# Kernel tuning notes

Measured on AMD Instinct MI355X. Metric: run time of the kernel, lower is better.

Reference implementation:

```python
import jax, jax.numpy as jnp
import numpy as np

N_NODES = 50000
N_EDGES = 800000
N_FEAT = 128
N_HID = 128
N_CLS = 40
BN_EPS = 1e-5


def setup_inputs() -> dict:
    key = jax.random.key(0)
    ks = jax.random.split(key, 8)
    return {
        "x": jax.random.normal(ks[0], (N_NODES, N_FEAT), dtype=jnp.float32),
        "edge_index": jax.random.randint(ks[1], (2, N_EDGES), 0, N_NODES, dtype=jnp.int64),
        "W1l": jax.random.normal(ks[2], (N_HID, N_FEAT), dtype=jnp.float32) / np.sqrt(N_FEAT),
        "b1": jnp.zeros((N_HID,), dtype=jnp.float32),
        "W1r": jax.random.normal(ks[3], (N_HID, N_FEAT), dtype=jnp.float32) / np.sqrt(N_FEAT),
        "gamma": jnp.ones((N_HID,), dtype=jnp.float32),
        "beta": jnp.zeros((N_HID,), dtype=jnp.float32),
        "run_mean": jax.random.normal(ks[4], (N_HID,), dtype=jnp.float32) * 0.1,
        "run_var": jax.random.uniform(ks[5], (N_HID,), dtype=jnp.float32) + 0.5,
        "W2l": jax.random.normal(ks[6], (N_CLS, N_HID), dtype=jnp.float32) / np.sqrt(N_HID),
        "b2": jnp.zeros((N_CLS,), dtype=jnp.float32),
        "W2r": jax.random.normal(ks[7], (N_CLS, N_HID), dtype=jnp.float32) / np.sqrt(N_HID),
    }


def _sage_conv(h, src, dst, n_nodes, inv_deg, Wl, bl, Wr):
    # mean-aggregate neighbor features at each destination node
    agg = jax.ops.segment_sum(h[src], dst, num_segments=n_nodes)  # [N, D]
    agg = agg * inv_deg[:, None]
    # PyG SAGEConv: lin_l(aggr) (with bias) + lin_r(x) (no bias)
    return agg @ Wl.T + bl + h @ Wr.T


def reference(x, edge_index, W1l, b1, W1r, gamma, beta, run_mean, run_var, W2l, b2, W2r):
    src, dst = edge_index[0], edge_index[1]
    n = x.shape[0]
    deg = jax.ops.segment_sum(jnp.ones_like(src, dtype=x.dtype), dst, num_segments=n)
    inv_deg = 1.0 / jnp.maximum(deg, 1.0)
    h = _sage_conv(x, src, dst, n, inv_deg, W1l, b1, W1r)
    # transition: ReLU -> BatchNorm1d (eval: running stats) -> Dropout (identity in eval)
    h = jnp.maximum(h, 0.0)
    h = (h - run_mean) * (gamma / jnp.sqrt(run_var + BN_EPS)) + beta
    out = _sage_conv(h, src, dst, n, inv_deg, W2l, b2, W2r)
    return out
```

## Files before the change

### kernel.cpp

```cpp
#include <hip/hip_runtime.h>

#define N_NODES 50000
#define N_EDGES 800000
#define N_FEAT 128
#define N_HID 128
#define N_CLS 40
#define BN_EPS 1e-5f

#define CSR_STRIDE 64
#define NXCD 8
#define P_NODES 6250
#define CSR_B 1024
#define CSR_BO 128
#define WPACK_B 84
#define XPACK_B 3125

typedef short bf16x8 __attribute__((ext_vector_type(8)));
typedef float f32x4 __attribute__((ext_vector_type(4)));

__device__ __forceinline__ unsigned bfpack(float a, float b) {
    unsigned ua = __float_as_uint(a), ub = __float_as_uint(b);
    ua = (ua + 0x7FFFu + ((ua >> 16) & 1u)) >> 16;
    ub = (ub + 0x7FFFu + ((ub >> 16) & 1u)) >> 16;
    return ua | (ub << 16);
}
__device__ __forceinline__ unsigned short bfr1(float a) {
    unsigned u = __float_as_uint(a);
    u = (u + 0x7FFFu + ((u >> 16) & 1u)) >> 16;
    return (unsigned short)u;
}
__device__ __forceinline__ float bflo(unsigned u) { return __uint_as_float(u << 16); }
__device__ __forceinline__ float bfhi(unsigned u) { return __uint_as_float(u & 0xFFFF0000u); }

__global__ __launch_bounds__(256) void degprep_kernel(
    const int* __restrict__ src, const int* __restrict__ dst,
    int* __restrict__ deg_i, unsigned short* __restrict__ csr_pad,
    const float* __restrict__ W1l, const float* __restrict__ W1r,
    const float* __restrict__ W2l, const float* __restrict__ W2r,
    const float* __restrict__ x, unsigned* __restrict__ WfA,
    unsigned* __restrict__ WfB, unsigned* __restrict__ x_bf16) {
    int b = blockIdx.x;
    int t = threadIdx.x;
    if (b < CSR_B) {
        const int p = b & (NXCD - 1);
        const int bo = b >> 3;
        const int plo = p * P_NODES;
        const int phi = plo + P_NODES;
        const int4* dst4 = (const int4*)dst;
        const int4* src4 = (const int4*)src;
        for (int c = bo; c * 2048 < N_EDGES; c += CSR_BO) {
            int e = c * 2048 + t * 8;
            if (e < N_EDGES) {
                int i4 = e >> 2;
                int4 da = dst4[i4];
                int4 db = dst4[i4 + 1];
                bool ka0 = (da.x >= plo) && (da.x < phi);
                bool ka1 = (da.y >= plo) && (da.y < phi);
                bool ka2 = (da.z >= plo) && (da.z < phi);
                bool ka3 = (da.w >= plo) && (da.w < phi);
                bool kb0 = (db.x >= plo) && (db.x < phi);
                bool kb1 = (db.y >= plo) && (db.y < phi);
                bool kb2 = (db.z >= plo) && (db.z < phi);
                bool kb3 = (db.w >= plo) && (db.w < phi);
                int4 sa = {0, 0, 0, 0}, sb = {0, 0, 0, 0};
                if (ka0 | ka1 | ka2 | ka3) sa = src4[i4];
                if (kb0 | kb1 | kb2 | kb3) sb = src4[i4 + 1];
                if (ka0) { int r = atomicAdd(&deg_i[da.x], 1);
                    if (r < CSR_STRIDE) csr_pad[da.x * CSR_STRIDE + r] = (unsigned short)sa.x; }
                if (ka1) { int r = atomicAdd(&deg_i[da.y], 1);
                    if (r < CSR_STRIDE) csr_pad[da.y * CSR_STRIDE + r] = (unsigned short)sa.y; }
                if (ka2) { int r = atomicAdd(&deg_i[da.z], 1);
                    if (r < CSR_STRIDE) csr_pad[da.z * CSR_STRIDE + r] = (unsigned short)sa.z; }
                if (ka3) { int r = atomicAdd(&deg_i[da.w], 1);
                    if (r < CSR_STRIDE) csr_pad[da.w * CSR_STRIDE + r] = (unsigned short)sa.w; }
                if (kb0) { int r = atomicAdd(&deg_i[db.x], 1);
                    if (r < CSR_STRIDE) csr_pad[db.x * CSR_STRIDE + r] = (unsigned short)sb.x; }
                if (kb1) { int r = atomicAdd(&deg_i[db.y], 1);
                    if (r < CSR_STRIDE) csr_pad[db.y * CSR_STRIDE + r] = (unsigned short)sb.y; }
                if (kb2) { int r = atomicAdd(&deg_i[db.z], 1);
                    if (r < CSR_STRIDE) csr_pad[db.z * CSR_STRIDE + r] = (unsigned short)sb.z; }
                if (kb3) { int r = atomicAdd(&deg_i[db.w], 1);
                    if (r < CSR_STRIDE) csr_pad[db.w * CSR_STRIDE + r] = (unsigned short)sb.w; }
            }
        }
        return;
    }
    int i = (b - CSR_B) * 256 + t;
    if (b < CSR_B + WPACK_B) {
        if (i < 16384) {
            int f = i >> 8, r = i & 255;
            int lane = r >> 2, u = r & 3;
            int phase = f >> 5, kc = (f >> 3) & 3, nt = f & 7;
            int k0 = phase * 128 + kc * 32 + (lane >> 4) * 8 + u * 2;
            int n = nt * 16 + (lane & 15);
            float w0, w1;
            if (k0 < 128) {
                w0 = W1l[n * 128 + k0];
                w1 = W1l[n * 128 + k0 + 1];
            } else {
                w0 = W1r[n * 128 + k0 - 128];
                w1 = W1r[n * 128 + k0 - 127];
            }
            WfA[i] = bfpack(w0, w1);
        } else if (i < 21504) {
            int j = i - 16384;
            int f = j >> 8, r = j & 255;
            int lane = r >> 2, u = r & 3;
            int kc = f / 5, nt = f % 5;
            int k0 = kc * 32 + (lane >> 4) * 8 + u * 2;
            int n = nt * 16 + (lane & 15);
            float w0, w1;
            if (n < 40) {
                w0 = W2l[n * 128 + k0];
                w1 = W2l[n * 128 + k0 + 1];
            } else {
                w0 = W2r[(n - 40) * 128 + k0];
                w1 = W2r[(n - 40) * 128 + k0 + 1];
            }
            WfB[j] = bfpack(w0, w1);
        }
    } else {
        int j = (b - CSR_B - WPACK_B) * 256 + t;
        if (j < 800000) {
            const float4* xf = (const float4*)x;
            float4 a = xf[(size_t)j * 2];
            float4 bq = xf[(size_t)j * 2 + 1];
            uint4 o;
            o.x = bfpack(a.x, a.y);
            o.y = bfpack(a.z, a.w);
            o.z = bfpack(bq.x, bq.y);
            o.w = bfpack(bq.z, bq.w);
            ((uint4*)x_bf16)[j] = o;
        }
    }
}

__global__ __launch_bounds__(256) void gather1_kernel(const unsigned short* __restrict__ csr_pad,
                                                      const int* __restrict__ deg_i,
                                                      const unsigned* __restrict__ x_bf16,
                                                      unsigned* __restrict__ agg1b) {
    int sg = threadIdx.x >> 4;
    int li = threadIdx.x & 15;
    int gid = blockIdx.x * 16 + sg;
    if (gid >= N_NODES) return;
    int n = min(deg_i[gid], CSR_STRIDE);
    int beg = gid * CSR_STRIDE;
    int end = beg + n;
    const uint4* xb = (const uint4*)x_bf16;
    float acc[8];
#pragma unroll
    for (int j = 0; j < 8; ++j) acc[j] = 0.f;

    int e = beg;
    for (; e + 7 < end; e += 8) {
        uint4 tv[8];
#pragma unroll
        for (int q = 0; q < 8; ++q) {
            int s = csr_pad[e + q];
            tv[q] = xb[(size_t)s * 16 + li];
        }
#pragma unroll
        for (int q = 0; q < 8; ++q) {
            acc[0] += bflo(tv[q].x); acc[1] += bfhi(tv[q].x);
            acc[2] += bflo(tv[q].y); acc[3] += bfhi(tv[q].y);
            acc[4] += bflo(tv[q].z); acc[5] += bfhi(tv[q].z);
            acc[6] += bflo(tv[q].w); acc[7] += bfhi(tv[q].w);
        }
    }
    if (e + 3 < end) {
        uint4 tv[4];
#pragma unroll
        for (int q = 0; q < 4; ++q) {
            int s = csr_pad[e + q];
            tv[q] = xb[(size_t)s * 16 + li];
        }
#pragma unroll
        for (int q = 0; q < 4; ++q) {
            acc[0] += bflo(tv[q].x); acc[1] += bfhi(tv[q].x);
            acc[2] += bflo(tv[q].y); acc[3] += bfhi(tv[q].y);
            acc[4] += bflo(tv[q].z); acc[5] += bfhi(tv[q].z);
            acc[6] += bflo(tv[q].w); acc[7] += bfhi(tv[q].w);
        }
        e += 4;
    }
    for (; e < end; ++e) {
        int s = csr_pad[e];
        uint4 t0 = xb[(size_t)s * 16 + li];
        acc[0] += bflo(t0.x); acc[1] += bfhi(t0.x);
        acc[2] += bflo(t0.y); acc[3] += bfhi(t0.y);
        acc[4] += bflo(t0.z); acc[5] += bfhi(t0.z);
        acc[6] += bflo(t0.w); acc[7] += bfhi(t0.w);
    }
    float inv = 1.0f / fmaxf((float)n, 1.0f);
    uint4 o;
    o.x = bfpack(acc[0] * inv, acc[1] * inv);
    o.y = bfpack(acc[2] * inv, acc[3] * inv);
    o.z = bfpack(acc[4] * inv, acc[5] * inv);
    o.w = bfpack(acc[6] * inv, acc[7] * inv);
    ((uint4*)agg1b)[(size_t)gid * 16 + li] = o;
}

__global__ __launch_bounds__(256) void gemm_fused_kernel(
    const unsigned* __restrict__ agg1b, const unsigned* __restrict__ xb,
    const unsigned* __restrict__ WfA, const unsigned* __restrict__ WfB,
    const float* __restrict__ b1,
    const float* __restrict__ gamma, const float* __restrict__ beta,
    const float* __restrict__ rmean, const float* __restrict__ rvar,
    unsigned short* __restrict__ z2s, float* __restrict__ p2) {
    __shared__ unsigned Asu[64 * 68];
    const int t = threadIdx.x;
    const int wid = __builtin_amdgcn_readfirstlane(t >> 6);
    const int lane = t & 63;
    const int li = lane & 15;
    const int quad = lane >> 4;
    const int mbase = blockIdx.x * 64;

    f32x4 dacc[8];
#pragma unroll
    for (int nt = 0; nt < 8; ++nt) dacc[nt] = (f32x4){0.f, 0.f, 0.f, 0.f};

    for (int phase = 0; phase < 2; ++phase) {
        const unsigned* __restrict__ A = phase ? xb : agg1b;
        __syncthreads();
#pragma unroll
        for (int i = 0; i < 4; ++i) {
            int e = i * 256 + t;
            int row = e >> 4, seg = e & 15;
            int rr = mbase + row;
            rr = (rr < N_NODES) ? rr : N_NODES - 1;
            uint4 v = ((const uint4*)A)[(size_t)rr * 16 + seg];
            *(uint4*)&Asu[row * 68 + seg * 4] = v;
        }
        __syncthreads();
        bf16x8 af[4];
#pragma unroll
        for (int kc = 0; kc < 4; ++kc)
            af[kc] = *(const bf16x8*)&Asu[(wid * 16 + li) * 68 + kc * 16 + quad * 4];

        const unsigned* __restrict__ Wp = WfA + phase * 8192;
#pragma unroll
        for (int nt = 0; nt < 8; ++nt) {
#pragma unroll
            for (int kc = 0; kc < 4; ++kc) {
                bf16x8 bfr = *(const bf16x8*)(Wp + (size_t)(kc * 8 + nt) * 256 + lane * 4);
                dacc[nt] = __builtin_amdgcn_mfma_f32_16x16x32_bf16(af[kc], bfr, dacc[nt], 0, 0, 0);
            }
        }
    }

    __syncthreads();
    unsigned short* Hs = (unsigned short*)Asu;
#pragma unroll
    for (int nt = 0; nt < 8; ++nt) {
        int cg = nt * 16 + li;
        float sc = gamma[cg] * rsqrtf(rvar[cg] + BN_EPS);
        float sh = fmaf(-rmean[cg], sc, beta[cg]);
        float bb = b1[cg];
#pragma unroll
        for (int r = 0; r < 4; ++r) {
            int row = wid * 16 + quad * 4 + r;
            float pre = dacc[nt][r] + bb;
            Hs[row * 136 + cg] = bfr1(fmaf(fmaxf(pre, 0.f), sc, sh));
        }
    }
    __syncthreads();

    bf16x8 af2[4];
#pragma unroll
    for (int kc = 0; kc < 4; ++kc)
        af2[kc] = *(const bf16x8*)&Asu[(wid * 16 + li) * 68 + kc * 16 + quad * 4];

    f32x4 d2[5];
#pragma unroll
    for (int nt = 0; nt < 5; ++nt) d2[nt] = (f32x4){0.f, 0.f, 0.f, 0.f};
#pragma unroll
    for (int nt = 0; nt < 5; ++nt) {
#pragma unroll
        for (int kc = 0; kc < 4; ++kc) {
            bf16x8 bfr = *(const bf16x8*)(WfB + (size_t)(kc * 5 + nt) * 256 + lane * 4);
            d2[nt] = __builtin_amdgcn_mfma_f32_16x16x32_bf16(af2[kc], bfr, d2[nt], 0, 0, 0);
        }
    }

#pragma unroll
    for (int nt = 0; nt < 5; ++nt) {
        int cg = nt * 16 + li;
#pragma unroll
        for (int r = 0; r < 4; ++r) {
            int row = mbase + wid * 16 + quad * 4 + r;
            if (row < N_NODES) {
                float vv = d2[nt][r];
                if (cg < 40) z2s[(size_t)row * 40 + cg] = bfr1(vv);
                else p2[(size_t)row * 40 + (cg - 40)] = vv;
            }
        }
    }
}

__global__ __launch_bounds__(256) void gather2_kernel(const unsigned short* __restrict__ csr_pad,
                                                      const int* __restrict__ deg_i,
                                                      const unsigned short* __restrict__ z2s,
                                                      const float* __restrict__ p2,
                                                      const float* __restrict__ b2,
                                                      float* __restrict__ out) {
    int t = threadIdx.x;
    int sub = t / 10;
    int li = t - sub * 10;
    if (sub >= 25) return;
    int gid = blockIdx.x * 25 + sub;
    if (gid >= N_NODES) return;
    int n = min(deg_i[gid], CSR_STRIDE);
    int beg = gid * CSR_STRIDE;
    int end = beg + n;
    const uint2* z2 = (const uint2*)z2s;
    float4 acc = {0.f, 0.f, 0.f, 0.f};
    int e = beg;
    for (; e + 7 < end; e += 8) {
        uint2 tv[8];
#pragma unroll
        for (int q = 0; q < 8; ++q) {
            int s = csr_pad[e + q];
            tv[q] = z2[(size_t)s * 10 + li];
        }
#pragma unroll
        for (int q = 0; q < 8; ++q) {
            acc.x += bflo(tv[q].x); acc.y += bfhi(tv[q].x);
            acc.z += bflo(tv[q].y); acc.w += bfhi(tv[q].y);
        }
    }
    if (e + 3 < end) {
        uint2 tv[4];
#pragma unroll
        for (int q = 0; q < 4; ++q) {
            int s = csr_pad[e + q];
            tv[q] = z2[(size_t)s * 10 + li];
        }
#pragma unroll
        for (int q = 0; q < 4; ++q) {
            acc.x += bflo(tv[q].x); acc.y += bfhi(tv[q].x);
            acc.z += bflo(tv[q].y); acc.w += bfhi(tv[q].y);
        }
        e += 4;
    }
    for (; e < end; ++e) {
        int s = csr_pad[e];
        uint2 t0 = z2[(size_t)s * 10 + li];
        acc.x += bflo(t0.x); acc.y += bfhi(t0.x);
        acc.z += bflo(t0.y); acc.w += bfhi(t0.y);
    }
    float inv = 1.0f / fmaxf((float)n, 1.0f);
    float4 p = ((const float4*)p2)[(size_t)gid * 10 + li];
    float4 bb = ((const float4*)b2)[li];
    float4 r;
    r.x = fmaf(acc.x, inv, p.x + bb.x);
    r.y = fmaf(acc.y, inv, p.y + bb.y);
    r.z = fmaf(acc.z, inv, p.z + bb.z);
    r.w = fmaf(acc.w, inv, p.w + bb.w);
    ((float4*)out)[(size_t)gid * 10 + li] = r;
}

extern "C" void kernel_launch(void* const* d_in, const int* in_sizes, int n_in,
                              void* d_out, int out_size, void* d_ws, size_t ws_size,
                              hipStream_t stream) {
    const float* x     = (const float*)d_in[0];
    const int*   ei    = (const int*)d_in[1];
    const float* W1l   = (const float*)d_in[2];
    const float* b1    = (const float*)d_in[3];
    const float* W1r   = (const float*)d_in[4];
    const float* gamma = (const float*)d_in[5];
    const float* beta  = (const float*)d_in[6];
    const float* rmean = (const float*)d_in[7];
    const float* rvar  = (const float*)d_in[8];
    const float* W2l   = (const float*)d_in[9];
    const float* b2    = (const float*)d_in[10];
    const float* W2r   = (const float*)d_in[11];
    float* out = (float*)d_out;

    int* deg_i              = (int*)d_ws;
    unsigned short* csr_pad = (unsigned short*)(deg_i + 50048);
    unsigned* WfA           = (unsigned*)(deg_i + 50048 + 1600000);
    unsigned* WfB           = WfA + 16384;
    unsigned* x_bf16        = WfB + 5120;
    unsigned* agg1b         = x_bf16 + 3200000;
    unsigned short* z2s     = (unsigned short*)(agg1b + (size_t)50048 * 64);
    float* p2               = (float*)(z2s + (size_t)50048 * 40);

    const int* src = ei;
    const int* dst = ei + N_EDGES;

    hipMemsetAsync(deg_i, 0, (size_t)50048 * sizeof(int), stream);

    degprep_kernel<<<CSR_B + WPACK_B + XPACK_B, 256, 0, stream>>>(
        src, dst, deg_i, csr_pad, W1l, W1r, W2l, W2r, x, WfA, WfB, x_bf16);

    gather1_kernel<<<(N_NODES + 15) / 16, 256, 0, stream>>>(csr_pad, deg_i, x_bf16, agg1b);

    gemm_fused_kernel<<<(N_NODES + 63) / 64, 256, 0, stream>>>(
        agg1b, x_bf16, WfA, WfB, b1, gamma, beta, rmean, rvar, z2s, p2);

    gather2_kernel<<<(N_NODES + 24) / 25, 256, 0, stream>>>(csr_pad, deg_i, z2s, p2, b2, out);
}
```

Measured before the change: 195.5 us.

## Store bf16 features segment-major and partition gather1 segments across XCDs

The bf16 copy of x and the layer-1 aggregate are now stored as 16 feature segments, each 16 bytes wide and laid out contiguously over all nodes, instead of row-major per node. gather1 assigns one node-segment per thread, and blockIdx&7 selects the segment pair, so each XCD's blocks touch only two segments of x. The intent is that each XCD's working set fits in its own L2, cutting cross-die and HBM traffic for the random neighbor gathers. The cost is that each gathered load becomes an isolated 16-byte access instead of a coalesced 256-byte row read, so cache-line utilisation drops. The GEMM tile load is updated to read the new layout.

```diff
diff --git a/kernel.cpp b/kernel.cpp
--- a/kernel.cpp
+++ b/kernel.cpp
@@ -14,6 +14,8 @@
 #define CSR_BO 128
 #define WPACK_B 84
 #define XPACK_B 3125
+#define SEG_N 50048
+#define G1_OB 391
 
 typedef short bf16x8 __attribute__((ext_vector_type(8)));
 typedef float f32x4 __attribute__((ext_vector_type(4)));
@@ -122,15 +124,17 @@
     } else {
         int j = (b - CSR_B - WPACK_B) * 256 + t;
         if (j < 800000) {
+            int seg = j / 50000;
+            int node = j - seg * 50000;
             const float4* xf = (const float4*)x;
-            float4 a = xf[(size_t)j * 2];
-            float4 bq = xf[(size_t)j * 2 + 1];
+            float4 a = xf[(size_t)node * 32 + seg * 2];
+            float4 bq = xf[(size_t)node * 32 + seg * 2 + 1];
             uint4 o;
             o.x = bfpack(a.x, a.y);
             o.y = bfpack(a.z, a.w);
             o.z = bfpack(bq.x, bq.y);
             o.w = bfpack(bq.z, bq.w);
-            ((uint4*)x_bf16)[j] = o;
+            ((uint4*)x_bf16)[(size_t)seg * SEG_N + node] = o;
         }
     }
 }
@@ -139,14 +143,17 @@
                                                       const int* __restrict__ deg_i,
                                                       const unsigned* __restrict__ x_bf16,
                                                       unsigned* __restrict__ agg1b) {
-    int sg = threadIdx.x >> 4;
-    int li = threadIdx.x & 15;
-    int gid = blockIdx.x * 16 + sg;
-    if (gid >= N_NODES) return;
-    int n = min(deg_i[gid], CSR_STRIDE);
-    int beg = gid * CSR_STRIDE;
+    int b = blockIdx.x;
+    int g = b & 7;
+    int o = b >> 3;
+    int t = threadIdx.x;
+    int node = o * 128 + (t & 127);
+    int seg = g + ((t >> 7) << 3);
+    const uint4* xs = (const uint4*)x_bf16 + (size_t)seg * SEG_N;
+
+    int n = min(deg_i[node], CSR_STRIDE);
+    int beg = node * CSR_STRIDE;
     int end = beg + n;
-    const uint4* xb = (const uint4*)x_bf16;
     float acc[8];
 #pragma unroll
     for (int j = 0; j < 8; ++j) acc[j] = 0.f;
@@ -157,7 +164,7 @@
 #pragma unroll
         for (int q = 0; q < 8; ++q) {
             int s = csr_pad[e + q];
-            tv[q] = xb[(size_t)s * 16 + li];
+            tv[q] = xs[s];
         }
 #pragma unroll
         for (int q = 0; q < 8; ++q) {
@@ -172,7 +179,7 @@
 #pragma unroll
         for (int q = 0; q < 4; ++q) {
             int s = csr_pad[e + q];
-            tv[q] = xb[(size_t)s * 16 + li];
+            tv[q] = xs[s];
         }
 #pragma unroll
         for (int q = 0; q < 4; ++q) {
@@ -185,19 +192,19 @@
     }
     for (; e < end; ++e) {
         int s = csr_pad[e];
-        uint4 t0 = xb[(size_t)s * 16 + li];
+        uint4 t0 = xs[s];
         acc[0] += bflo(t0.x); acc[1] += bfhi(t0.x);
         acc[2] += bflo(t0.y); acc[3] += bfhi(t0.y);
         acc[4] += bflo(t0.z); acc[5] += bfhi(t0.z);
         acc[6] += bflo(t0.w); acc[7] += bfhi(t0.w);
     }
     float inv = 1.0f / fmaxf((float)n, 1.0f);
-    uint4 o;
-    o.x = bfpack(acc[0] * inv, acc[1] * inv);
-    o.y = bfpack(acc[2] * inv, acc[3] * inv);
-    o.z = bfpack(acc[4] * inv, acc[5] * inv);
-    o.w = bfpack(acc[6] * inv, acc[7] * inv);
-    ((uint4*)agg1b)[(size_t)gid * 16 + li] = o;
+    uint4 o4;
+    o4.x = bfpack(acc[0] * inv, acc[1] * inv);
+    o4.y = bfpack(acc[2] * inv, acc[3] * inv);
+    o4.z = bfpack(acc[4] * inv, acc[5] * inv);
+    o4.w = bfpack(acc[6] * inv, acc[7] * inv);
+    ((uint4*)agg1b)[(size_t)seg * SEG_N + node] = o4;
 }
 
 __global__ __launch_bounds__(256) void gemm_fused_kernel(
@@ -225,10 +232,10 @@
 #pragma unroll
         for (int i = 0; i < 4; ++i) {
             int e = i * 256 + t;
-            int row = e >> 4, seg = e & 15;
+            int seg = e >> 6, row = e & 63;
             int rr = mbase + row;
             rr = (rr < N_NODES) ? rr : N_NODES - 1;
-            uint4 v = ((const uint4*)A)[(size_t)rr * 16 + seg];
+            uint4 v = ((const uint4*)A)[(size_t)seg * SEG_N + rr];
             *(uint4*)&Asu[row * 68 + seg * 4] = v;
         }
         __syncthreads();
@@ -381,8 +388,8 @@
     unsigned* WfA           = (unsigned*)(deg_i + 50048 + 1600000);
     unsigned* WfB           = WfA + 16384;
     unsigned* x_bf16        = WfB + 5120;
-    unsigned* agg1b         = x_bf16 + 3200000;
-    unsigned short* z2s     = (unsigned short*)(agg1b + (size_t)50048 * 64);
+    unsigned* agg1b         = x_bf16 + (size_t)16 * SEG_N * 4;
+    unsigned short* z2s     = (unsigned short*)(agg1b + (size_t)16 * SEG_N * 4);
     float* p2               = (float*)(z2s + (size_t)50048 * 40);
 
     const int* src = ei;
@@ -393,7 +400,7 @@
     degprep_kernel<<<CSR_B + WPACK_B + XPACK_B, 256, 0, stream>>>(
         src, dst, deg_i, csr_pad, W1l, W1r, W2l, W2r, x, WfA, WfB, x_bf16);
 
-    gather1_kernel<<<(N_NODES + 15) / 16, 256, 0, stream>>>(csr_pad, deg_i, x_bf16, agg1b);
+    gather1_kernel<<<8 * G1_OB, 256, 0, stream>>>(csr_pad, deg_i, x_bf16, agg1b);
 
     gemm_fused_kernel<<<(N_NODES + 63) / 64, 256, 0, stream>>>(
         agg1b, x_bf16, WfA, WfB, b1, gamma, beta, rmean, rvar, z2s, p2);
```

Result: slower. 241.4 us (+23.5%).

## Fuse layer-1 gather into the dense GEMM kernel with 16-row tiles

Applied to the files above, without the earlier changes.

Merges the neighbor-mean gather and the fused two-GEMM/BN kernel into one kernel. Each 256-thread block gathers 16 nodes, stages the aggregate and the self features in shared memory, and its four waves split the output column tiles of both MFMA GEMMs. This removes the write and reread of the intermediate aggregate buffer and one kernel launch. In exchange each block now computes only 16 rows, so weight fragments are reloaded four times as often and the second GEMM is unevenly split across waves.

```diff
diff --git a/kernel.cpp b/kernel.cpp
--- a/kernel.cpp
+++ b/kernel.cpp
@@ -135,29 +135,42 @@
     }
 }
 
-__global__ __launch_bounds__(256) void gather1_kernel(const unsigned short* __restrict__ csr_pad,
-                                                      const int* __restrict__ deg_i,
-                                                      const unsigned* __restrict__ x_bf16,
-                                                      unsigned* __restrict__ agg1b) {
-    int sg = threadIdx.x >> 4;
-    int li = threadIdx.x & 15;
-    int gid = blockIdx.x * 16 + sg;
-    if (gid >= N_NODES) return;
+__global__ __launch_bounds__(256) void gg_kernel(
+    const unsigned short* __restrict__ csr_pad, const int* __restrict__ deg_i,
+    const unsigned* __restrict__ x_bf16,
+    const unsigned* __restrict__ WfA, const unsigned* __restrict__ WfB,
+    const float* __restrict__ b1,
+    const float* __restrict__ gamma, const float* __restrict__ beta,
+    const float* __restrict__ rmean, const float* __restrict__ rvar,
+    unsigned short* __restrict__ z2s, float* __restrict__ p2) {
+    __shared__ unsigned Asu0[16 * 68];
+    __shared__ unsigned Asu1[16 * 68];
+    const int t = threadIdx.x;
+    const int wid = __builtin_amdgcn_readfirstlane(t >> 6);
+    const int lane = t & 63;
+    const int li = lane & 15;
+    const int quad = lane >> 4;
+    const int sg = t >> 4;
+    const int gl = t & 15;
+    const int tb = blockIdx.x * 16;
+    const uint4* xb4 = (const uint4*)x_bf16;
+
+    uint4 xs = xb4[(size_t)(tb + sg) * 16 + gl];
+
+    int gid = tb + sg;
     int n = min(deg_i[gid], CSR_STRIDE);
     int beg = gid * CSR_STRIDE;
     int end = beg + n;
-    const uint4* xb = (const uint4*)x_bf16;
     float acc[8];
 #pragma unroll
     for (int j = 0; j < 8; ++j) acc[j] = 0.f;
-
     int e = beg;
     for (; e + 7 < end; e += 8) {
         uint4 tv[8];
 #pragma unroll
         for (int q = 0; q < 8; ++q) {
             int s = csr_pad[e + q];
-            tv[q] = xb[(size_t)s * 16 + li];
+            tv[q] = xb4[(size_t)s * 16 + gl];
         }
 #pragma unroll
         for (int q = 0; q < 8; ++q) {
@@ -172,7 +185,7 @@
 #pragma unroll
         for (int q = 0; q < 4; ++q) {
             int s = csr_pad[e + q];
-            tv[q] = xb[(size_t)s * 16 + li];
+            tv[q] = xb4[(size_t)s * 16 + gl];
         }
 #pragma unroll
         for (int q = 0; q < 4; ++q) {
@@ -185,7 +198,7 @@
     }
     for (; e < end; ++e) {
         int s = csr_pad[e];
-        uint4 t0 = xb[(size_t)s * 16 + li];
+        uint4 t0 = xb4[(size_t)s * 16 + gl];
         acc[0] += bflo(t0.x); acc[1] += bfhi(t0.x);
         acc[2] += bflo(t0.y); acc[3] += bfhi(t0.y);
         acc[4] += bflo(t0.z); acc[5] += bfhi(t0.z);
@@ -197,70 +210,50 @@
     o.y = bfpack(acc[2] * inv, acc[3] * inv);
     o.z = bfpack(acc[4] * inv, acc[5] * inv);
     o.w = bfpack(acc[6] * inv, acc[7] * inv);
-    ((uint4*)agg1b)[(size_t)gid * 16 + li] = o;
-}
-
-__global__ __launch_bounds__(256) void gemm_fused_kernel(
-    const unsigned* __restrict__ agg1b, const unsigned* __restrict__ xb,
-    const unsigned* __restrict__ WfA, const unsigned* __restrict__ WfB,
-    const float* __restrict__ b1,
-    const float* __restrict__ gamma, const float* __restrict__ beta,
-    const float* __restrict__ rmean, const float* __restrict__ rvar,
-    unsigned short* __restrict__ z2s, float* __restrict__ p2) {
-    __shared__ unsigned Asu[64 * 68];
-    const int t = threadIdx.x;
-    const int wid = __builtin_amdgcn_readfirstlane(t >> 6);
-    const int lane = t & 63;
-    const int li = lane & 15;
-    const int quad = lane >> 4;
-    const int mbase = blockIdx.x * 64;
-
-    f32x4 dacc[8];
-#pragma unroll
-    for (int nt = 0; nt < 8; ++nt) dacc[nt] = (f32x4){0.f, 0.f, 0.f, 0.f};
-
-    for (int phase = 0; phase < 2; ++phase) {
-        const unsigned* __restrict__ A = phase ? xb : agg1b;
-        __syncthreads();
-#pragma unroll
-        for (int i = 0; i < 4; ++i) {
-            int e = i * 256 + t;
-            int row = e >> 4, seg = e & 15;
-            int rr = mbase + row;
-            rr = (rr < N_NODES) ? rr : N_NODES - 1;
-            uint4 v = ((const uint4*)A)[(size_t)rr * 16 + seg];
-            *(uint4*)&Asu[row * 68 + seg * 4] = v;
-        }
-        __syncthreads();
-        bf16x8 af[4];
-#pragma unroll
-        for (int kc = 0; kc < 4; ++kc)
-            af[kc] = *(const bf16x8*)&Asu[(wid * 16 + li) * 68 + kc * 16 + quad * 4];
-
-        const unsigned* __restrict__ Wp = WfA + phase * 8192;
-#pragma unroll
-        for (int nt = 0; nt < 8; ++nt) {
-#pragma unroll
-            for (int kc = 0; kc < 4; ++kc) {
-                bf16x8 bfr = *(const bf16x8*)(Wp + (size_t)(kc * 8 + nt) * 256 + lane * 4);
-                dacc[nt] = __builtin_amdgcn_mfma_f32_16x16x32_bf16(af[kc], bfr, dacc[nt], 0, 0, 0);
-            }
-        }
-    }
-
+
+    *(uint4*)&Asu1[sg * 68 + gl * 4] = xs;
+    *(uint4*)&Asu0[sg * 68 + gl * 4] = o;
     __syncthreads();
-    unsigned short* Hs = (unsigned short*)Asu;
-#pragma unroll
-    for (int nt = 0; nt < 8; ++nt) {
-        int cg = nt * 16 + li;
-        float sc = gamma[cg] * rsqrtf(rvar[cg] + BN_EPS);
-        float sh = fmaf(-rmean[cg], sc, beta[cg]);
-        float bb = b1[cg];
+
+    bf16x8 af0[4], af1[4];
+#pragma unroll
+    for (int kc = 0; kc < 4; ++kc) {
+        af0[kc] = *(const bf16x8*)&Asu0[li * 68 + kc * 16 + quad * 4];
+        af1[kc] = *(const bf16x8*)&Asu1[li * 68 + kc * 16 + quad * 4];
+    }
+
+    f32x4 dacc[2];
+#pragma unroll
+    for (int j = 0; j < 2; ++j) dacc[j] = (f32x4){0.f, 0.f, 0.f, 0.f};
+#pragma unroll
+    for (int j = 0; j < 2; ++j) {
+        int nt = wid * 2 + j;
+#pragma unroll
+        for (int kc = 0; kc < 4; ++kc) {
+            bf16x8 bfr = *(const bf16x8*)(WfA + (size_t)(kc * 8 + nt) * 256 + lane * 4);
+            dacc[j] = __builtin_amdgcn_mfma_f32_16x16x32_bf16(af0[kc], bfr, dacc[j], 0, 0, 0);
+        }
+#pragma unroll
+        for (int kc = 0; kc < 4; ++kc) {
+            bf16x8 bfr = *(const bf16x8*)(WfA + 8192 + (size_t)(kc * 8 + nt) * 256 + lane * 4);
+            dacc[j] = __builtin_amdgcn_mfma_f32_16x16x32_bf16(af1[kc], bfr, dacc[j], 0, 0, 0);
+        }
+    }
+    __syncthreads();
+
+    unsigned short* Hs = (unsigned short*)Asu0;
+#pragma unroll
+    for (int j = 0; j < 2; ++j) {
+        int nt = wid * 2 + j;
+        int cgc = nt * 16 + li;
+        float sc = gamma[cgc] * rsqrtf(rvar[cgc] + BN_EPS);
+        float sh = fmaf(-rmean[cgc], sc, beta[cgc]);
+        float bb = b1[cgc];
 #pragma unroll
         for (int r = 0; r < 4; ++r) {
-            int row = wid * 16 + quad * 4 + r;
-            float pre = dacc[nt][r] + bb;
-            Hs[row * 136 + cg] = bfr1(fmaf(fmaxf(pre, 0.f), sc, sh));
+            int row = quad * 4 + r;
+            float pre = dacc[j][r] + bb;
+            Hs[row * 136 + cgc] = bfr1(fmaf(fmaxf(pre, 0.f), sc, sh));
         }
     }
     __syncthreads();
@@ -268,31 +261,29 @@
     bf16x8 af2[4];
 #pragma unroll
     for (int kc = 0; kc < 4; ++kc)
-        af2[kc] = *(const bf16x8*)&Asu[(wid * 16 + li) * 68 + kc * 16 + quad * 4];
-
-    f32x4 d2[5];
-#pragma unroll
-    for (int nt = 0; nt < 5; ++nt) d2[nt] = (f32x4){0.f, 0.f, 0.f, 0.f};
-#pragma unroll
-    for (int nt = 0; nt < 5; ++nt) {
+        af2[kc] = *(const bf16x8*)&Asu0[li * 68 + kc * 16 + quad * 4];
+
+    int nNT = (wid == 0) ? 2 : 1;
+    f32x4 d2[2];
+#pragma unroll
+    for (int j = 0; j < 2; ++j) d2[j] = (f32x4){0.f, 0.f, 0.f, 0.f};
+    for (int j = 0; j < nNT; ++j) {
+        int nt = (j == 0) ? wid : 4;
 #pragma unroll
         for (int kc = 0; kc < 4; ++kc) {
             bf16x8 bfr = *(const bf16x8*)(WfB + (size_t)(kc * 5 + nt) * 256 + lane * 4);
-            d2[nt] = __builtin_amdgcn_mfma_f32_16x16x32_bf16(af2[kc], bfr, d2[nt], 0, 0, 0);
-        }
-    }
-
-#pragma unroll
-    for (int nt = 0; nt < 5; ++nt) {
-        int cg = nt * 16 + li;
+            d2[j] = __builtin_amdgcn_mfma_f32_16x16x32_bf16(af2[kc], bfr, d2[j], 0, 0, 0);
+        }
+    }
+    for (int j = 0; j < nNT; ++j) {
+        int nt = (j == 0) ? wid : 4;
+        int cgc = nt * 16 + li;
 #pragma unroll
         for (int r = 0; r < 4; ++r) {
-            int row = mbase + wid * 16 + quad * 4 + r;
-            if (row < N_NODES) {
-                float vv = d2[nt][r];
-                if (cg < 40) z2s[(size_t)row * 40 + cg] = bfr1(vv);
-                else p2[(size_t)row * 40 + (cg - 40)] = vv;
-            }
+            int row = tb + quad * 4 + r;
+            float vv = d2[j][r];
+            if (cgc < 40) z2s[(size_t)row * 40 + cgc] = bfr1(vv);
+            else p2[(size_t)row * 40 + (cgc - 40)] = vv;
         }
     }
 }
@@ -381,8 +372,7 @@
     unsigned* WfA           = (unsigned*)(deg_i + 50048 + 1600000);
     unsigned* WfB           = WfA + 16384;
     unsigned* x_bf16        = WfB + 5120;
-    unsigned* agg1b         = x_bf16 + 3200000;
-    unsigned short* z2s     = (unsigned short*)(agg1b + (size_t)50048 * 64);
+    unsigned short* z2s     = (unsigned short*)(x_bf16 + 3200000);
     float* p2               = (float*)(z2s + (size_t)50048 * 40);
 
     const int* src = ei;
@@ -393,10 +383,8 @@
     degprep_kernel<<<CSR_B + WPACK_B + XPACK_B, 256, 0, stream>>>(
         src, dst, deg_i, csr_pad, W1l, W1r, W2l, W2r, x, WfA, WfB, x_bf16);
 
-    gather1_kernel<<<(N_NODES + 15) / 16, 256, 0, stream>>>(csr_pad, deg_i, x_bf16, agg1b);
-
-    gemm_fused_kernel<<<(N_NODES + 63) / 64, 256, 0, stream>>>(
-        agg1b, x_bf16, WfA, WfB, b1, gamma, beta, rmean, rvar, z2s, p2);
+    gg_kernel<<<N_NODES / 16, 256, 0, stream>>>(
+        csr_pad, deg_i, x_bf16, WfA, WfB, b1, gamma, beta, rmean, rvar, z2s, p2);
 
     gather2_kernel<<<(N_NODES + 24) / 25, 256, 0, stream>>>(csr_pad, deg_i, z2s, p2, b2, out);
 }
```

Measured after the change: 187.3 us. 1.04x faster.
